# Optimization experiments

Hardware: AMD Instinct MI355X
Metric: run time of the kernel (lower is better)

Reference implementation:

```python
import jax, jax.numpy as jnp
import numpy as np

NEG_NUM = -10000.0


def setup_inputs() -> dict:
    key = jax.random.key(0)
    ks = jax.random.split(key, 7)
    B, L, M, H, A = 32, 2048, 512, 512, 256
    memory = jax.random.normal(ks[0], (B, L, M), dtype=jnp.float32)
    hidden = jax.random.normal(ks[1], (B, H), dtype=jnp.float32)
    mask = jax.random.randint(ks[2], (B, L), 0, 2, dtype=jnp.int32)
    # ensure no fully-masked row (softmax well-defined)
    mask = mask.at[:, 0].set(1)
    # nn.Linear params: W1 (A, M+H), b1 (A,), W2 (1, A), b2 (1,)
    lim1 = 1.0 / np.sqrt(M + H)
    W1 = jax.random.uniform(ks[3], (A, M + H), jnp.float32, -lim1, lim1)
    b1 = jax.random.uniform(ks[4], (A,), jnp.float32, -lim1, lim1)
    lim2 = 1.0 / np.sqrt(A)
    W2 = jax.random.uniform(ks[5], (1, A), jnp.float32, -lim2, lim2)
    b2 = jax.random.uniform(ks[6], (1,), jnp.float32, -lim2, lim2)
    return {"memory": memory, "hidden": hidden, "mask": mask,
            "W1": W1, "b1": b1, "W2": W2, "b2": b2}


def reference(memory, hidden, mask, W1, b1, W2, b2):
    # memory: (B, L, M), hidden: (B, H)
    M = memory.shape[-1]
    # Split W1 so we never materialize the concat: equivalent to
    # Linear(cat([memory, hidden_expanded])) since cat@W1^T = mem@W1m^T + hid@W1h^T
    W1m, W1h = W1[:, :M], W1[:, M:]
    proj = (jnp.einsum('blm,am->bla', memory, W1m)
            + jnp.einsum('bh,ah->ba', hidden, W1h)[:, None, :]
            + b1)                                   # (B, L, A)
    score = jnp.einsum('bla,a->bl', jnp.tanh(proj), W2[0]) + b2[0]  # (B, L)
    score = jnp.where(mask == 0, NEG_NUM, score)
    p_memory = jax.nn.softmax(score, axis=-1)        # (B, L)
    expected_memory = jnp.einsum('bl,blm->bm', p_memory, memory)  # (B, M)
    return expected_memory, p_memory
```

## Files before the change

### kernel.cpp

```cpp
#include <hip/hip_runtime.h>
#include <hip/hip_bf16.h>

constexpr int Bb = 32;
constexpr int Ll = 2048;
constexpr int Mm = 512;
constexpr int Hh = 512;
constexpr int Aa = 256;

typedef __attribute__((ext_vector_type(4))) float f32x4;
typedef __attribute__((ext_vector_type(8))) short short8;
typedef __attribute__((ext_vector_type(4))) unsigned short ushort4v;

__device__ __forceinline__ unsigned short f2bf(float f) {
    __hip_bfloat16 h = __float2bfloat16(f);
    return *reinterpret_cast<unsigned short*>(&h);
}

__global__ void k_convert_w1m(const float* __restrict__ W1,
                              unsigned short* __restrict__ W1mb) {
    int i = blockIdx.x * 256 + threadIdx.x;
    int a  = i >> 7;
    int mq = (i & 127) << 2;
    f32x4 v = *reinterpret_cast<const f32x4*>(W1 + (size_t)a * (Mm + Hh) + mq);
    ushort4v o;
    o[0] = f2bf(v[0]); o[1] = f2bf(v[1]); o[2] = f2bf(v[2]); o[3] = f2bf(v[3]);
    *reinterpret_cast<ushort4v*>(W1mb + (size_t)a * Mm + mq) = o;
}

__global__ void k_hb(const float* __restrict__ hidden, const float* __restrict__ W1,
                     const float* __restrict__ b1, float* __restrict__ hb) {
    int b  = blockIdx.x >> 2;
    int hc = blockIdx.x & 3;
    int a  = threadIdx.x;
    __shared__ float sh[128];
    if (threadIdx.x < 128) sh[threadIdx.x] = hidden[b * Hh + hc * 128 + threadIdx.x];
    __syncthreads();
    const float* wrow = W1 + (size_t)a * (Mm + Hh) + Mm + hc * 128;
    float acc = (hc == 0) ? b1[a] : 0.f;
    #pragma unroll 8
    for (int h = 0; h < 128; h += 4) {
        f32x4 w = *reinterpret_cast<const f32x4*>(wrow + h);
        acc += w[0] * sh[h] + w[1] * sh[h + 1] + w[2] * sh[h + 2] + w[3] * sh[h + 3];
    }
    atomicAdd(&hb[b * Aa + a], acc);
}

__launch_bounds__(256, 2)
__global__ void k_score(const float* __restrict__ mem,
                        const unsigned short* __restrict__ W1mb,
                        const float* __restrict__ hb, const float* __restrict__ W2,
                        float* __restrict__ score) {
    const int wave = threadIdx.x >> 6;
    const int lane = threadIdx.x & 63;
    const int g = lane >> 4;
    const int r = lane & 15;
    const int rowbase = blockIdx.x * 128 + wave * 32;
    const int b = rowbase >> 11;

    f32x4 acc[2][16];
    #pragma unroll
    for (int rt = 0; rt < 2; rt++)
        #pragma unroll
        for (int ct = 0; ct < 16; ct++)
            acc[rt][ct] = (f32x4){0.f, 0.f, 0.f, 0.f};

    const float* ap0 = mem + (size_t)(rowbase + r) * Mm + g * 8;
    const float* ap1 = ap0 + (size_t)16 * Mm;
    const unsigned short* bp0 = W1mb + (size_t)r * Mm + g * 8;

    for (int ks = 0; ks < 16; ++ks) {
        const int ko = ks * 32;
        short8 af0, af1;
        {
            f32x4 lo = *reinterpret_cast<const f32x4*>(ap0 + ko);
            f32x4 hi = *reinterpret_cast<const f32x4*>(ap0 + ko + 4);
            af0[0] = (short)f2bf(lo[0]); af0[1] = (short)f2bf(lo[1]);
            af0[2] = (short)f2bf(lo[2]); af0[3] = (short)f2bf(lo[3]);
            af0[4] = (short)f2bf(hi[0]); af0[5] = (short)f2bf(hi[1]);
            af0[6] = (short)f2bf(hi[2]); af0[7] = (short)f2bf(hi[3]);
        }
        {
            f32x4 lo = *reinterpret_cast<const f32x4*>(ap1 + ko);
            f32x4 hi = *reinterpret_cast<const f32x4*>(ap1 + ko + 4);
            af1[0] = (short)f2bf(lo[0]); af1[1] = (short)f2bf(lo[1]);
            af1[2] = (short)f2bf(lo[2]); af1[3] = (short)f2bf(lo[3]);
            af1[4] = (short)f2bf(hi[0]); af1[5] = (short)f2bf(hi[1]);
            af1[6] = (short)f2bf(hi[2]); af1[7] = (short)f2bf(hi[3]);
        }
        #pragma unroll
        for (int half = 0; half < 2; ++half) {
            short8 bf[8];
            #pragma unroll
            for (int j = 0; j < 8; ++j) {
                int ct = half * 8 + j;
                bf[j] = *reinterpret_cast<const short8*>(bp0 + (size_t)ct * 16 * Mm + ko);
            }
            #pragma unroll
            for (int j = 0; j < 8; ++j) {
                int ct = half * 8 + j;
                acc[0][ct] = __builtin_amdgcn_mfma_f32_16x16x32_bf16(af0, bf[j], acc[0][ct], 0, 0, 0);
                acc[1][ct] = __builtin_amdgcn_mfma_f32_16x16x32_bf16(af1, bf[j], acc[1][ct], 0, 0, 0);
            }
        }
    }

    float s0[4] = {0.f, 0.f, 0.f, 0.f};
    float s1[4] = {0.f, 0.f, 0.f, 0.f};
    #pragma unroll
    for (int ct = 0; ct < 16; ++ct) {
        int a = ct * 16 + r;
        float hba = hb[b * Aa + a];
        float w2a = W2[a];
        #pragma unroll
        for (int reg = 0; reg < 4; ++reg) {
            {
                float pr = acc[0][ct][reg] + hba;
                float e = __expf(2.f * pr);
                float t = (e - 1.f) * __builtin_amdgcn_rcpf(e + 1.f);
                s0[reg] += t * w2a;
            }
            {
                float pr = acc[1][ct][reg] + hba;
                float e = __expf(2.f * pr);
                float t = (e - 1.f) * __builtin_amdgcn_rcpf(e + 1.f);
                s1[reg] += t * w2a;
            }
        }
    }
    #pragma unroll
    for (int off = 1; off < 16; off <<= 1) {
        #pragma unroll
        for (int reg = 0; reg < 4; ++reg) {
            s0[reg] += __shfl_xor(s0[reg], off, 64);
            s1[reg] += __shfl_xor(s1[reg], off, 64);
        }
    }
    if (r == 0) {
        #pragma unroll
        for (int reg = 0; reg < 4; ++reg) {
            score[rowbase + g * 4 + reg]      = s0[reg];
            score[rowbase + 16 + g * 4 + reg] = s1[reg];
        }
    }
}

__global__ void k_softmax(const float* __restrict__ score, const int* __restrict__ mask,
                          float* __restrict__ p) {
    __shared__ float smx[4];
    __shared__ float ssm[4];
    int b = blockIdx.x, tid = threadIdx.x;
    float v[8]; int mk[8];
    #pragma unroll
    for (int i = 0; i < 8; i++) {
        int l = i * 256 + tid;
        v[i]  = score[b * Ll + l];
        mk[i] = mask[b * Ll + l];
    }
    float mx = -1e30f;
    #pragma unroll
    for (int i = 0; i < 8; i++) if (mk[i]) mx = fmaxf(mx, v[i]);
    for (int off = 1; off < 64; off <<= 1) mx = fmaxf(mx, __shfl_xor(mx, off, 64));
    if ((tid & 63) == 0) smx[tid >> 6] = mx;
    __syncthreads();
    mx = fmaxf(fmaxf(smx[0], smx[1]), fmaxf(smx[2], smx[3]));

    float e[8]; float s = 0.f;
    #pragma unroll
    for (int i = 0; i < 8; i++) { e[i] = mk[i] ? __expf(v[i] - mx) : 0.f; s += e[i]; }
    for (int off = 1; off < 64; off <<= 1) s += __shfl_xor(s, off, 64);
    if ((tid & 63) == 0) ssm[tid >> 6] = s;
    __syncthreads();
    s = ssm[0] + ssm[1] + ssm[2] + ssm[3];
    float inv = 1.f / s;
    #pragma unroll
    for (int i = 0; i < 8; i++) p[b * Ll + i * 256 + tid] = e[i] * inv;
}

__global__ void k_expected(const float* __restrict__ mem, const float* __restrict__ p,
                           float* __restrict__ out) {
    int b  = blockIdx.x >> 4;
    int ch = blockIdx.x & 15;
    int m4 = (threadIdx.x & 127) << 2;
    int ls = threadIdx.x >> 7;
    f32x4 acc = (f32x4){0.f, 0.f, 0.f, 0.f};
    const float* base = mem + (size_t)b * Ll * Mm + (size_t)ch * 128 * Mm;
    const float* pb = p + b * Ll + ch * 128;
    for (int il = ls; il < 128; il += 2) {
        float pv = pb[il];
        f32x4 mv = *reinterpret_cast<const f32x4*>(base + (size_t)il * Mm + m4);
        acc += mv * pv;
    }
    float* o = out + b * Mm + m4;
    atomicAdd(o + 0, acc[0]);
    atomicAdd(o + 1, acc[1]);
    atomicAdd(o + 2, acc[2]);
    atomicAdd(o + 3, acc[3]);
}

extern "C" void kernel_launch(void* const* d_in, const int* in_sizes, int n_in,
                              void* d_out, int out_size, void* d_ws, size_t ws_size,
                              hipStream_t stream) {
    const float* memory = (const float*)d_in[0];
    const float* hidden = (const float*)d_in[1];
    const int*   mask   = (const int*)d_in[2];
    const float* W1     = (const float*)d_in[3];
    const float* b1     = (const float*)d_in[4];
    const float* W2     = (const float*)d_in[5];
    float* out = (float*)d_out;

    unsigned short* W1mb = (unsigned short*)d_ws;
    float* hb    = (float*)((char*)d_ws + 256 * 1024);
    float* score = (float*)((char*)d_ws + 256 * 1024 + 32 * 1024);
    float* p = out + Bb * Mm;

    hipMemsetAsync(out, 0, (size_t)Bb * Mm * sizeof(float), stream);
    hipMemsetAsync(hb, 0, (size_t)Bb * Aa * sizeof(float), stream);

    k_convert_w1m<<<128, 256, 0, stream>>>(W1, W1mb);
    k_hb<<<128, 256, 0, stream>>>(hidden, W1, b1, hb);
    k_score<<<512, 256, 0, stream>>>(memory, W1mb, hb, W2, score);
    k_softmax<<<32, 256, 0, stream>>>(score, mask, p);
    k_expected<<<512, 256, 0, stream>>>(memory, p, out);
}
```

Baseline: 290.1 us.

## Stage score GEMM operands in double-buffered LDS and remove atomics in expected sum

The score kernel now stages bf16 W1m tiles through LDS using direct global-to-LDS loads, in a ks-blocked layout written by the conversion kernel. It also converts memory rows to bf16 once into double-buffered LDS, so B fragments are no longer re-read from global memory by every wave. Blocks shrink to 64 rows with a 4-block occupancy target and twice as many blocks. The expected-memory kernel gives each block a 32-column slice over the full sequence and reduces in shared memory, dropping the atomics and the output memset. The trade-off is lower per-thread parallelism per column chunk in k_expected and a barrier on every k-step in k_score.

```diff
diff --git a/kernel.cpp b/kernel.cpp
--- a/kernel.cpp
+++ b/kernel.cpp
@@ -14,6 +14,18 @@
 __device__ __forceinline__ unsigned short f2bf(float f) {
     __hip_bfloat16 h = __float2bfloat16(f);
     return *reinterpret_cast<unsigned short*>(&h);
+}
+
+__device__ __forceinline__ ushort4v cvt4(f32x4 v) {
+    ushort4v o;
+    o[0] = f2bf(v[0]); o[1] = f2bf(v[1]); o[2] = f2bf(v[2]); o[3] = f2bf(v[3]);
+    return o;
+}
+
+__device__ __forceinline__ void gload_lds16(const void* g, void* l) {
+    __builtin_amdgcn_global_load_lds(
+        (const __attribute__((address_space(1))) unsigned int*)g,
+        (__attribute__((address_space(3))) unsigned int*)l, 16, 0, 0);
 }
 
 __global__ void k_convert_w1m(const float* __restrict__ W1,
@@ -22,9 +34,9 @@
     int a  = i >> 7;
     int mq = (i & 127) << 2;
     f32x4 v = *reinterpret_cast<const f32x4*>(W1 + (size_t)a * (Mm + Hh) + mq);
-    ushort4v o;
-    o[0] = f2bf(v[0]); o[1] = f2bf(v[1]); o[2] = f2bf(v[2]); o[3] = f2bf(v[3]);
-    *reinterpret_cast<ushort4v*>(W1mb + (size_t)a * Mm + mq) = o;
+    int ks = mq >> 5;
+    int kb = mq & 31;
+    *reinterpret_cast<ushort4v*>(W1mb + (size_t)ks * (Aa * 32) + a * 32 + kb) = cvt4(v);
 }
 
 __global__ void k_hb(const float* __restrict__ hidden, const float* __restrict__ W1,
@@ -45,67 +57,74 @@
     atomicAdd(&hb[b * Aa + a], acc);
 }
 
-__launch_bounds__(256, 2)
+__launch_bounds__(256, 4)
 __global__ void k_score(const float* __restrict__ mem,
                         const unsigned short* __restrict__ W1mb,
                         const float* __restrict__ hb, const float* __restrict__ W2,
                         float* __restrict__ score) {
-    const int wave = threadIdx.x >> 6;
-    const int lane = threadIdx.x & 63;
+    __shared__ unsigned short ldsA[2][64 * 32];
+    __shared__ unsigned short ldsB[2][256 * 32];
+
+    const int tid  = threadIdx.x;
+    const int wave = tid >> 6;
+    const int lane = tid & 63;
     const int g = lane >> 4;
     const int r = lane & 15;
-    const int rowbase = blockIdx.x * 128 + wave * 32;
-    const int b = rowbase >> 11;
-
-    f32x4 acc[2][16];
-    #pragma unroll
-    for (int rt = 0; rt < 2; rt++)
-        #pragma unroll
-        for (int ct = 0; ct < 16; ct++)
-            acc[rt][ct] = (f32x4){0.f, 0.f, 0.f, 0.f};
-
-    const float* ap0 = mem + (size_t)(rowbase + r) * Mm + g * 8;
-    const float* ap1 = ap0 + (size_t)16 * Mm;
-    const unsigned short* bp0 = W1mb + (size_t)r * Mm + g * 8;
+    const int blockRow = blockIdx.x * 64;
+    const int b = blockRow >> 11;
+
+    f32x4 acc[16];
+    #pragma unroll
+    for (int ct = 0; ct < 16; ct++) acc[ct] = (f32x4){0.f, 0.f, 0.f, 0.f};
+
+    const int c0 = tid, c1 = tid + 256;
+    const float* gA0 = mem + (size_t)(blockRow + (c0 >> 3)) * Mm + (c0 & 7) * 4;
+    const float* gA1 = mem + (size_t)(blockRow + (c1 >> 3)) * Mm + (c1 & 7) * 4;
+    const char* gB = (const char*)W1mb;
+
+    {
+        #pragma unroll
+        for (int j = 0; j < 4; ++j)
+            gload_lds16(gB + (size_t)(wave * 4 + j) * 1024 + lane * 16,
+                        &ldsB[0][(wave * 4 + j) * 512]);
+        f32x4 a0 = *reinterpret_cast<const f32x4*>(gA0);
+        f32x4 a1 = *reinterpret_cast<const f32x4*>(gA1);
+        *reinterpret_cast<ushort4v*>(&ldsA[0][c0 * 4]) = cvt4(a0);
+        *reinterpret_cast<ushort4v*>(&ldsA[0][c1 * 4]) = cvt4(a1);
+    }
+    __syncthreads();
 
     for (int ks = 0; ks < 16; ++ks) {
-        const int ko = ks * 32;
-        short8 af0, af1;
-        {
-            f32x4 lo = *reinterpret_cast<const f32x4*>(ap0 + ko);
-            f32x4 hi = *reinterpret_cast<const f32x4*>(ap0 + ko + 4);
-            af0[0] = (short)f2bf(lo[0]); af0[1] = (short)f2bf(lo[1]);
-            af0[2] = (short)f2bf(lo[2]); af0[3] = (short)f2bf(lo[3]);
-            af0[4] = (short)f2bf(hi[0]); af0[5] = (short)f2bf(hi[1]);
-            af0[6] = (short)f2bf(hi[2]); af0[7] = (short)f2bf(hi[3]);
-        }
-        {
-            f32x4 lo = *reinterpret_cast<const f32x4*>(ap1 + ko);
-            f32x4 hi = *reinterpret_cast<const f32x4*>(ap1 + ko + 4);
-            af1[0] = (short)f2bf(lo[0]); af1[1] = (short)f2bf(lo[1]);
-            af1[2] = (short)f2bf(lo[2]); af1[3] = (short)f2bf(lo[3]);
-            af1[4] = (short)f2bf(hi[0]); af1[5] = (short)f2bf(hi[1]);
-            af1[6] = (short)f2bf(hi[2]); af1[7] = (short)f2bf(hi[3]);
-        }
-        #pragma unroll
-        for (int half = 0; half < 2; ++half) {
-            short8 bf[8];
+        const int cur = ks & 1, nxt = cur ^ 1;
+        f32x4 a0, a1;
+        if (ks < 15) {
+            const int ko = (ks + 1) * 32;
             #pragma unroll
-            for (int j = 0; j < 8; ++j) {
-                int ct = half * 8 + j;
-                bf[j] = *reinterpret_cast<const short8*>(bp0 + (size_t)ct * 16 * Mm + ko);
-            }
+            for (int j = 0; j < 4; ++j)
+                gload_lds16(gB + (size_t)(ks + 1) * 16384 + (wave * 4 + j) * 1024 + lane * 16,
+                            &ldsB[nxt][(wave * 4 + j) * 512]);
+            a0 = *reinterpret_cast<const f32x4*>(gA0 + ko);
+            a1 = *reinterpret_cast<const f32x4*>(gA1 + ko);
+        }
+        short8 af = *reinterpret_cast<const short8*>(&ldsA[cur][(wave * 16 + r) * 32 + g * 8]);
+        #pragma unroll
+        for (int h = 0; h < 4; ++h) {
+            short8 bf[4];
             #pragma unroll
-            for (int j = 0; j < 8; ++j) {
-                int ct = half * 8 + j;
-                acc[0][ct] = __builtin_amdgcn_mfma_f32_16x16x32_bf16(af0, bf[j], acc[0][ct], 0, 0, 0);
-                acc[1][ct] = __builtin_amdgcn_mfma_f32_16x16x32_bf16(af1, bf[j], acc[1][ct], 0, 0, 0);
-            }
-        }
-    }
-
-    float s0[4] = {0.f, 0.f, 0.f, 0.f};
-    float s1[4] = {0.f, 0.f, 0.f, 0.f};
+            for (int j = 0; j < 4; ++j)
+                bf[j] = *reinterpret_cast<const short8*>(&ldsB[cur][((h * 4 + j) * 16 + r) * 32 + g * 8]);
+            #pragma unroll
+            for (int j = 0; j < 4; ++j)
+                acc[h * 4 + j] = __builtin_amdgcn_mfma_f32_16x16x32_bf16(af, bf[j], acc[h * 4 + j], 0, 0, 0);
+        }
+        if (ks < 15) {
+            *reinterpret_cast<ushort4v*>(&ldsA[nxt][c0 * 4]) = cvt4(a0);
+            *reinterpret_cast<ushort4v*>(&ldsA[nxt][c1 * 4]) = cvt4(a1);
+        }
+        __syncthreads();
+    }
+
+    float s[4] = {0.f, 0.f, 0.f, 0.f};
     #pragma unroll
     for (int ct = 0; ct < 16; ++ct) {
         int a = ct * 16 + r;
@@ -113,34 +132,21 @@
         float w2a = W2[a];
         #pragma unroll
         for (int reg = 0; reg < 4; ++reg) {
-            {
-                float pr = acc[0][ct][reg] + hba;
-                float e = __expf(2.f * pr);
-                float t = (e - 1.f) * __builtin_amdgcn_rcpf(e + 1.f);
-                s0[reg] += t * w2a;
-            }
-            {
-                float pr = acc[1][ct][reg] + hba;
-                float e = __expf(2.f * pr);
-                float t = (e - 1.f) * __builtin_amdgcn_rcpf(e + 1.f);
-                s1[reg] += t * w2a;
-            }
+            float pr = acc[ct][reg] + hba;
+            float e = __expf(2.f * pr);
+            float t = (e - 1.f) * __builtin_amdgcn_rcpf(e + 1.f);
+            s[reg] += t * w2a;
         }
     }
     #pragma unroll
     for (int off = 1; off < 16; off <<= 1) {
         #pragma unroll
-        for (int reg = 0; reg < 4; ++reg) {
-            s0[reg] += __shfl_xor(s0[reg], off, 64);
-            s1[reg] += __shfl_xor(s1[reg], off, 64);
-        }
+        for (int reg = 0; reg < 4; ++reg) s[reg] += __shfl_xor(s[reg], off, 64);
     }
     if (r == 0) {
         #pragma unroll
-        for (int reg = 0; reg < 4; ++reg) {
-            score[rowbase + g * 4 + reg]      = s0[reg];
-            score[rowbase + 16 + g * 4 + reg] = s1[reg];
-        }
+        for (int reg = 0; reg < 4; ++reg)
+            score[blockRow + wave * 16 + g * 4 + reg] = s[reg];
     }
 }
 
@@ -178,23 +184,28 @@
 
 __global__ void k_expected(const float* __restrict__ mem, const float* __restrict__ p,
                            float* __restrict__ out) {
+    __shared__ f32x4 sred[32][8];
     int b  = blockIdx.x >> 4;
-    int ch = blockIdx.x & 15;
-    int m4 = (threadIdx.x & 127) << 2;
-    int ls = threadIdx.x >> 7;
+    int mc = blockIdx.x & 15;
+    int mi = threadIdx.x & 7;
+    int ls = threadIdx.x >> 3;
+    const float* base = mem + (size_t)b * Ll * Mm + mc * 32 + mi * 4;
+    const float* pb = p + b * Ll;
     f32x4 acc = (f32x4){0.f, 0.f, 0.f, 0.f};
-    const float* base = mem + (size_t)b * Ll * Mm + (size_t)ch * 128 * Mm;
-    const float* pb = p + b * Ll + ch * 128;
-    for (int il = ls; il < 128; il += 2) {
+    for (int il = ls; il < Ll; il += 32) {
         float pv = pb[il];
-        f32x4 mv = *reinterpret_cast<const f32x4*>(base + (size_t)il * Mm + m4);
+        f32x4 mv = *reinterpret_cast<const f32x4*>(base + (size_t)il * Mm);
         acc += mv * pv;
     }
-    float* o = out + b * Mm + m4;
-    atomicAdd(o + 0, acc[0]);
-    atomicAdd(o + 1, acc[1]);
-    atomicAdd(o + 2, acc[2]);
-    atomicAdd(o + 3, acc[3]);
+    sred[ls][mi] = acc;
+    __syncthreads();
+    #pragma unroll
+    for (int s = 16; s > 0; s >>= 1) {
+        if (ls < s) sred[ls][mi] += sred[ls + s][mi];
+        __syncthreads();
+    }
+    if (ls == 0)
+        *reinterpret_cast<f32x4*>(out + b * Mm + mc * 32 + mi * 4) = sred[0][mi];
 }
 
 extern "C" void kernel_launch(void* const* d_in, const int* in_sizes, int n_in,
@@ -213,12 +224,11 @@
     float* score = (float*)((char*)d_ws + 256 * 1024 + 32 * 1024);
     float* p = out + Bb * Mm;
 
-    hipMemsetAsync(out, 0, (size_t)Bb * Mm * sizeof(float), stream);
     hipMemsetAsync(hb, 0, (size_t)Bb * Aa * sizeof(float), stream);
 
     k_convert_w1m<<<128, 256, 0, stream>>>(W1, W1mb);
     k_hb<<<128, 256, 0, stream>>>(hidden, W1, b1, hb);
-    k_score<<<512, 256, 0, stream>>>(memory, W1mb, hb, W2, score);
+    k_score<<<1024, 256, 0, stream>>>(memory, W1mb, hb, W2, score);
     k_softmax<<<32, 256, 0, stream>>>(score, mask, p);
     k_expected<<<512, 256, 0, stream>>>(memory, p, out);
 }
```

Result: faster. 244.2 us (-15.8%).
